# Optimization experiments

Hardware: AMD Instinct MI355X
Metric: run time of the kernel (lower is better)

## Reference

```python
import jax, jax.numpy as jnp
import numpy as np

KERNEL_SIZE = 16
B, L = 64, 8192
HIDDEN, OUT_CH = 64, 8


def setup_inputs() -> dict:
    key = jax.random.key(0)
    k1, k2, k3 = jax.random.split(key, 3)
    x = jax.random.normal(k1, (B, L), dtype=jnp.float32)
    W1 = jax.random.normal(k2, (KERNEL_SIZE, HIDDEN), dtype=jnp.float32) * (1.0 / np.sqrt(KERNEL_SIZE))
    b1 = jnp.zeros((HIDDEN,), dtype=jnp.float32)
    W2 = jax.random.normal(k3, (HIDDEN, OUT_CH), dtype=jnp.float32) * (1.0 / np.sqrt(HIDDEN))
    b2 = jnp.zeros((OUT_CH,), dtype=jnp.float32)
    return {"x": x, "W1": W1, "b1": b1, "W2": W2, "b2": b2}


def reference(x, W1, b1, W2, b2):
    k = KERNEL_SIZE
    n_batch, length = x.shape
    out_len = length - k + 1  # stride=1 per module's reshape logic
    # im2col: windows[b, w, j] = x[b, w + j]
    idx = jnp.arange(out_len)[:, None] + jnp.arange(k)[None, :]  # [out_len, k]
    windows = x[:, idx]                                          # [B, out_len, k]
    rows = windows.reshape(-1, k)                                # [B*out_len, k]
    # kernel_module: MLP per window row
    h = jnp.tanh(rows @ W1 + b1)                                 # [B*out_len, H]
    y = h @ W2 + b2                                              # [B*out_len, out_ch]
    # faithful to torch: out.reshape(n_batch, -1, output_shape)
    return y.reshape(n_batch, -1, out_len)                       # [B, out_ch, out_len]
```

## Files before the change

### kernel.cpp

```cpp
#include <hip/hip_runtime.h>
#include <hip/hip_bf16.h>

#define KS 16
#define HID 64
#define OC 8
#define LEN 8192
#define OUT_LEN (LEN - KS + 1)
#define BATCH 64
#define TPW 4
#define STRIPS 32

typedef __attribute__((ext_vector_type(8))) short short8;
typedef __attribute__((ext_vector_type(4))) float f32x4;
typedef __attribute__((ext_vector_type(4), aligned(4))) float f32x4u;

static __device__ inline short bf16s(float f) {
    union { __hip_bfloat16 h; short s; } u;
    u.h = __float2bfloat16(f);
    return u.s;
}

__global__ __launch_bounds__(256, 4) void conv_mlp_mfma(
    const float* __restrict__ x, const float* __restrict__ W1,
    const float* __restrict__ b1, const float* __restrict__ W2,
    const float* __restrict__ b2, float* __restrict__ out)
{
    const int lane = threadIdx.x & 63;
    const int wave = threadIdx.x >> 6;
    const int col  = lane & 15;
    const int g    = lane >> 4;

    const int batch = blockIdx.x >> 5;
    const int strip = blockIdx.x & 31;
    const int tile0 = strip * 16 + wave * TPW;

    short8 a1[4];
#pragma unroll
    for (int T = 0; T < 4; ++T) {
#pragma unroll
        for (int e = 0; e < 8; ++e) {
            float v = 0.0f;
            if (g < 2)                 v = W1[(8 * g + e) * HID + 16 * T + col];
            else if (g == 2 && e == 0) v = b1[16 * T + col];
            a1[T][e] = bf16s(v);
        }
    }

    short8 a2[2];
#pragma unroll
    for (int t = 0; t < 2; ++t) {
#pragma unroll
        for (int e = 0; e < 8; ++e) {
            int j = 32 * t + 16 * (e >> 2) + 4 * g + (e & 3);
            float v = (col < OC) ? W2[j * OC + col] : 0.0f;
            a2[t][e] = bf16s(v);
        }
    }

    f32x4 b2v;
#pragma unroll
    for (int r = 0; r < 4; ++r) b2v[r] = b2[(4 * g + r) & (OC - 1)];

    const float* xb = x + batch * LEN;
    float* ob = out + (size_t)batch * OUT_LEN * OC;

    for (int t8 = 0; t8 < TPW; ++t8) {
        const int p0 = (tile0 + t8) * 16;
        const int p  = p0 + col;

        short8 b1f = {0, 0, 0, 0, 0, 0, 0, 0};
        if (g < 2) {
            int b0 = p + 8 * g;
            b0 = b0 > (LEN - 8) ? (LEN - 8) : b0;
            f32x4u lo = *(const f32x4u*)(xb + b0);
            f32x4u hi = *(const f32x4u*)(xb + b0 + 4);
#pragma unroll
            for (int e = 0; e < 4; ++e) b1f[e]     = bf16s(lo[e]);
#pragma unroll
            for (int e = 0; e < 4; ++e) b1f[4 + e] = bf16s(hi[e]);
        } else if (g == 2) {
            b1f[0] = (short)0x3F80;
        }

        f32x4 acc[4] = {{0,0,0,0},{0,0,0,0},{0,0,0,0},{0,0,0,0}};
#pragma unroll
        for (int T = 0; T < 4; ++T)
            acc[T] = __builtin_amdgcn_mfma_f32_16x16x32_bf16(a1[T], b1f, acc[T], 0, 0, 0);

        short8 hb[2];
#pragma unroll
        for (int T = 0; T < 4; ++T) {
#pragma unroll
            for (int r = 0; r < 4; ++r) {
                float h  = acc[T][r];
                float e2 = __builtin_amdgcn_exp2f(h * 2.885390081777927f);
                float tn = fmaf(-2.0f, __builtin_amdgcn_rcpf(e2 + 1.0f), 1.0f);
                hb[T >> 1][4 * (T & 1) + r] = bf16s(tn);
            }
        }

        f32x4 accY = b2v;
        accY = __builtin_amdgcn_mfma_f32_16x16x32_bf16(a2[0], hb[0], accY, 0, 0, 0);
        accY = __builtin_amdgcn_mfma_f32_16x16x32_bf16(a2[1], hb[1], accY, 0, 0, 0);

        if (g < 2 && p < OUT_LEN) {
            *(f32x4*)(ob + (size_t)p * OC + 4 * g) = accY;
        }
    }
}

extern "C" void kernel_launch(void* const* d_in, const int* in_sizes, int n_in,
                              void* d_out, int out_size, void* d_ws, size_t ws_size,
                              hipStream_t stream) {
    const float* x  = (const float*)d_in[0];
    const float* W1 = (const float*)d_in[1];
    const float* b1 = (const float*)d_in[2];
    const float* W2 = (const float*)d_in[3];
    const float* b2 = (const float*)d_in[4];
    float* out = (float*)d_out;

    dim3 grid(BATCH * STRIPS);
    conv_mlp_mfma<<<grid, 256, 0, stream>>>(x, W1, b1, W2, b2, out);
}
```

Before: 20.78 us.

## Double tiles per wave, prefetch next x tile, and use nontemporal output stores

Each wave now handles 8 tiles instead of 4 and the grid is halved, so the per-block weight setup (W1/W2 bf16 packing) is amortized over more work. The loop is unrolled and the x window for the next tile is loaded into registers one iteration early to hide global load latency behind MFMA and tanh work. Output stores become nontemporal to avoid polluting cache with streamed results. Trade-offs: fewer blocks (1024) may reduce latency hiding, the full unroll raises register pressure, and all lanes now issue x loads, including g>=2 lanes whose values are discarded.

```diff
diff --git a/kernel.cpp b/kernel.cpp
--- a/kernel.cpp
+++ b/kernel.cpp
@@ -7,8 +7,8 @@
 #define LEN 8192
 #define OUT_LEN (LEN - KS + 1)
 #define BATCH 64
-#define TPW 4
-#define STRIPS 32
+#define TPW 8
+#define STRIPS 16
 
 typedef __attribute__((ext_vector_type(8))) short short8;
 typedef __attribute__((ext_vector_type(4))) float f32x4;
@@ -18,6 +18,13 @@
     union { __hip_bfloat16 h; short s; } u;
     u.h = __float2bfloat16(f);
     return u.s;
+}
+
+static __device__ inline void nt_store4(float* p, f32x4 v) {
+    __builtin_nontemporal_store(v.x, p + 0);
+    __builtin_nontemporal_store(v.y, p + 1);
+    __builtin_nontemporal_store(v.z, p + 2);
+    __builtin_nontemporal_store(v.w, p + 3);
 }
 
 __global__ __launch_bounds__(256, 4) void conv_mlp_mfma(
@@ -30,9 +37,9 @@
     const int col  = lane & 15;
     const int g    = lane >> 4;
 
-    const int batch = blockIdx.x >> 5;
-    const int strip = blockIdx.x & 31;
-    const int tile0 = strip * 16 + wave * TPW;
+    const int batch = blockIdx.x >> 4;
+    const int strip = blockIdx.x & 15;
+    const int tile0 = strip * 32 + wave * TPW;
 
     short8 a1[4];
 #pragma unroll
@@ -64,22 +71,35 @@
     const float* xb = x + batch * LEN;
     float* ob = out + (size_t)batch * OUT_LEN * OC;
 
+    const int boff = col + 8 * (g & 1);
+
+    int nb = tile0 * 16 + boff;
+    nb = nb > (LEN - 8) ? (LEN - 8) : nb;
+    f32x4 nlo = *(const f32x4u*)(xb + nb);
+    f32x4 nhi = *(const f32x4u*)(xb + nb + 4);
+
+#pragma unroll
     for (int t8 = 0; t8 < TPW; ++t8) {
         const int p0 = (tile0 + t8) * 16;
         const int p  = p0 + col;
 
-        short8 b1f = {0, 0, 0, 0, 0, 0, 0, 0};
-        if (g < 2) {
-            int b0 = p + 8 * g;
+        f32x4 clo = nlo, chi = nhi;
+        if (t8 + 1 < TPW) {
+            int b0 = (p0 + 16) + boff;
             b0 = b0 > (LEN - 8) ? (LEN - 8) : b0;
-            f32x4u lo = *(const f32x4u*)(xb + b0);
-            f32x4u hi = *(const f32x4u*)(xb + b0 + 4);
+            nlo = *(const f32x4u*)(xb + b0);
+            nhi = *(const f32x4u*)(xb + b0 + 4);
+        }
+
+        short8 b1f;
 #pragma unroll
-            for (int e = 0; e < 4; ++e) b1f[e]     = bf16s(lo[e]);
+        for (int e = 0; e < 4; ++e) b1f[e]     = bf16s(clo[e]);
 #pragma unroll
-            for (int e = 0; e < 4; ++e) b1f[4 + e] = bf16s(hi[e]);
-        } else if (g == 2) {
-            b1f[0] = (short)0x3F80;
+        for (int e = 0; e < 4; ++e) b1f[4 + e] = bf16s(chi[e]);
+        if (g >= 2) {
+            short8 z = {0, 0, 0, 0, 0, 0, 0, 0};
+            if (g == 2) z[0] = (short)0x3F80;
+            b1f = z;
         }
 
         f32x4 acc[4] = {{0,0,0,0},{0,0,0,0},{0,0,0,0},{0,0,0,0}};
@@ -104,7 +124,7 @@
         accY = __builtin_amdgcn_mfma_f32_16x16x32_bf16(a2[1], hb[1], accY, 0, 0, 0);
 
         if (g < 2 && p < OUT_LEN) {
-            *(f32x4*)(ob + (size_t)p * OC + 4 * g) = accY;
+            nt_store4(ob + (size_t)p * OC + 4 * g, accY);
         }
     }
 }
```

Measured after the change: 20.17 us. 1.03x faster.
